# Optimization experiments

Hardware: AMD Instinct MI355X
Metric: run time of the kernel (lower is better)

Reference implementation:

```python
import jax, jax.numpy as jnp
import numpy as np
from jax import lax

N_CLS = 3
ALPHA = 2
NMS = True


def _make_level(key, B, A, D, H, W, P, counts):
    k1, k2, k3, k4, k5 = jax.random.split(key, 5)
    C = N_CLS * A
    logit = jax.random.normal(k1, (B, C, D, H, W), dtype=jnp.float32)
    # valid positive coords use d,h,w >= 1 so padded writes to (0,0,0,0) never collide
    a = jax.random.randint(k2, (B, P), 0, A)
    d = jax.random.randint(k3, (B, P), 1, D)
    h = jax.random.randint(k4, (B, P), 1, H)
    w = jax.random.randint(k5, (B, P), 1, W)
    labels = jax.random.randint(jax.random.fold_in(key, 7), (B, P), 0, N_CLS)
    valid = jnp.arange(P)[None, :] < jnp.asarray(counts)[:, None]  # [B,P]
    coord = jnp.stack([a, d, h, w], axis=-1)
    coord = jnp.where(valid[..., None], coord, -1).astype(jnp.int32)
    # ground-truth prob map: -1 = negative, class id (float) at positive voxels
    prob_gt = -jnp.ones((B, A, D, H, W), dtype=jnp.float32)
    cs = jnp.where(valid[..., None], coord, 0)
    b_idx = jnp.arange(B)[:, None]
    vals = jnp.where(valid, labels.astype(jnp.float32), -1.0)
    prob_gt = prob_gt.at[b_idx, cs[..., 0], cs[..., 1], cs[..., 2], cs[..., 3]].set(vals)
    return logit, prob_gt, coord


def setup_inputs() -> dict:
    key = jax.random.key(0)
    kA, kB = jax.random.split(key)
    logit0, prob_gt0, coord0 = _make_level(kA, 4, 3, 64, 64, 64, 128, [128, 64, 32, 0])
    logit1, prob_gt1, coord1 = _make_level(kB, 4, 3, 32, 32, 32, 128, [64, 16, 8, 128])
    weight_cls = jnp.array([1.0, 1.5, 2.0], dtype=jnp.float32)
    return {
        "logit0": logit0, "logit1": logit1,
        "prob_gt0": prob_gt0, "prob_gt1": prob_gt1,
        "coord0": coord0, "coord1": coord1,
        "weight_cls": weight_cls,
    }


def _level_loss(logit, prob_gt, coord_gt, weight_cls):
    B, C, D, H, W = logit.shape
    A = C // N_CLS
    logit = logit.reshape(B, N_CLS, A, D, H, W)
    logp = jax.nn.log_softmax(logit, axis=1)
    nll = -logp                      # [B,N_cls,A,D,H,W]
    prob = jnp.exp(logp)
    nll_neg = nll[:, 0]              # [B,A,D,H,W]
    prob_neg = prob[:, 0]
    negmask = (prob_gt == -1).astype(logit.dtype)
    if NMS:
        mp = lax.reduce_window(nll_neg, -jnp.inf, lax.max,
                               (1, 1, 3, 3, 3), (1, 1, 1, 1, 1),
                               [(0, 0), (0, 0), (1, 1), (1, 1), (1, 1)])
        negmask = negmask * lax.stop_gradient((mp == nll_neg).astype(logit.dtype))
    w_neg = (1.0 - lax.stop_gradient(prob_neg)) ** ALPHA * negmask
    loss_neg = jnp.sum(nll_neg * w_neg)
    count_neg = jnp.sum(w_neg)
    # positives: ragged coord gather, masked instead of per-sample python loop
    valid = coord_gt[:, :, 0] > -1                       # [B,P]
    c = jnp.where(valid[..., None], coord_gt, 0)         # safe coords
    a, d, h, w = c[..., 0], c[..., 1], c[..., 2], c[..., 3]
    b_idx = jnp.arange(B)[:, None]
    cls = prob_gt[b_idx, a, d, h, w].astype(jnp.int32)   # class id at positives
    cls = jnp.where(valid, cls, 0)
    p_t = prob[b_idx, cls, a, d, h, w]
    nll_t = nll[b_idx, cls, a, d, h, w]
    w_pos = ((1.0 - lax.stop_gradient(p_t)) ** ALPHA
             * weight_cls[cls] * valid.astype(logit.dtype))
    loss_pos = jnp.sum(nll_t * w_pos)
    count_pos = jnp.sum(w_pos)
    return loss_pos, loss_neg, count_pos, count_neg


def reference(logit0, logit1, prob_gt0, prob_gt1, coord0, coord1, weight_cls):
    lp0, ln0, cp0, cn0 = _level_loss(logit0, prob_gt0, coord0, weight_cls)
    lp1, ln1, cp1, cn1 = _level_loss(logit1, prob_gt1, coord1, weight_cls)
    return jnp.stack([lp0 + lp1, ln0 + ln1, cp0 + cp1, cn0 + cn1])
```

## Files before the change

### kernel.cpp

```cpp
#include <hip/hip_runtime.h>
#include <math.h>

#define NEG_INF (-INFINITY)

__device__ __forceinline__ float nll3(float l0, float l1, float l2) {
    float m = fmaxf(l0, fmaxf(l1, l2));
    float e0 = __expf(l0 - m);
    float e1 = __expf(l1 - m);
    float e2 = __expf(l2 - m);
    return __logf(e0 + e1 + e2) - (l0 - m);
}

template<int W, int NR, int TD, int D, int H>
__device__ void neg_strip_v(int uid, int lane,
                            const float* __restrict__ logit,
                            const float* __restrict__ pg,
                            float2* __restrict__ slot) {
    constexpr int LR = W / 4;
    constexpr int NG = 64 / LR;
    constexpr int NI = NR + 2;
    constexpr int HG = H / NR;
    constexpr int DT = D / TD;
    const int q = lane % LR;
    const int g = lane / LR;

    int t = uid;
    const int hg = t % HG; t /= HG;
    const int dt = t % DT; t /= DT;
    const int ba = t;
    const int a = ba % 3, b = ba / 3;
    const int h0 = hg * NR, d0 = dt * TD;

    const long S = (long)D * H * W;
    const float* lb  = logit + ((long)b * 9 + a) * S;
    const long  cs   = 3 * S;
    const float* pgb = pg + (long)ba * S;

    const int jrow = h0 - 1 + g;
    const bool hv = (jrow >= 0) && (jrow < H) && (g < NI);
    const int hcl = min(max(jrow, 0), H - 1);
    const int rowoff = hcl * W + 4 * q;
    const int prowoff = (h0 + min(g, NR - 1)) * W + 4 * q;

    float4 c0, c1v, c2, n0, n1, n2, pgn;
    bool dvc = (d0 - 1 >= 0);
    {
        const float* p = lb + (long)max(d0 - 1, 0) * (H * W) + rowoff;
        c0  = *(const float4*)(p);
        c1v = *(const float4*)(p + cs);
        c2  = *(const float4*)(p + 2 * cs);
    }

    float vm0[4], vm1[4], cc1[4], pgc[4];
#pragma unroll
    for (int i = 0; i < 4; ++i) {
        vm0[i] = NEG_INF; vm1[i] = NEG_INF; cc1[i] = 0.f; pgc[i] = 0.f;
    }

    float loss = 0.f, cnt = 0.f;

#pragma unroll
    for (int s = 0; s <= TD + 1; ++s) {
        const int d = d0 - 1 + s;
        const bool dvn = (s <= TD - 1) || (d + 1 < D);
        if (s <= TD) {
            const float* p = lb + (long)min(d + 1, D - 1) * (H * W) + rowoff;
            n0 = *(const float4*)(p);
            n1 = *(const float4*)(p + cs);
            n2 = *(const float4*)(p + 2 * cs);
            pgn = *(const float4*)(pgb + (long)min(max(d, 0), D - 1) * (H * W)
                                   + prowoff);
        }

        float nvv[4];
        {
            const bool vv = dvc && hv;
            nvv[0] = vv ? nll3(c0.x, c1v.x, c2.x) : NEG_INF;
            nvv[1] = vv ? nll3(c0.y, c1v.y, c2.y) : NEG_INF;
            nvv[2] = vv ? nll3(c0.z, c1v.z, c2.z) : NEG_INF;
            nvv[3] = vv ? nll3(c0.w, c1v.w, c2.w) : NEG_INF;
        }

        float le = __shfl(nvv[3], lane - 1);
        float re = __shfl(nvv[0], lane + 1);
        le = (q == 0)      ? NEG_INF : le;
        re = (q == LR - 1) ? NEG_INF : re;
        float rm[4];
        rm[0] = fmaxf(le,     fmaxf(nvv[0], nvv[1]));
        rm[1] = fmaxf(nvv[0], fmaxf(nvv[1], nvv[2]));
        rm[2] = fmaxf(nvv[1], fmaxf(nvv[2], nvv[3]));
        rm[3] = fmaxf(nvv[2], fmaxf(nvv[3], re));

        float rmA[4], rmB[4], ctr[4];
#pragma unroll
        for (int i = 0; i < 4; ++i) {
            rmA[i] = __shfl(rm[i],  lane + LR);
            rmB[i] = __shfl(rm[i],  lane + 2 * LR);
            ctr[i] = __shfl(nvv[i], lane + LR);
        }

#pragma unroll
        for (int i = 0; i < 4; ++i) {
            float hw2 = fmaxf(rm[i], fmaxf(rmA[i], rmB[i]));
            if (s >= 2 && g < NR && pgc[i] == -1.0f) {
                float mp = fmaxf(vm0[i], fmaxf(vm1[i], hw2));
                if (mp == cc1[i]) {
                    float pn = __expf(-cc1[i]);
                    float wn = (1.f - pn) * (1.f - pn);
                    loss += cc1[i] * wn;
                    cnt  += wn;
                }
            }
            vm0[i] = vm1[i]; vm1[i] = hw2; cc1[i] = ctr[i];
        }
        pgc[0] = pgn.x; pgc[1] = pgn.y; pgc[2] = pgn.z; pgc[3] = pgn.w;
        dvc = dvn;
        c0 = n0; c1v = n1; c2 = n2;
    }

#pragma unroll
    for (int off = 32; off > 0; off >>= 1) {
        loss += __shfl_down(loss, off);
        cnt  += __shfl_down(cnt, off);
    }
    if (lane == 0) slot[uid] = make_float2(loss, cnt);
}

__device__ void pos_wave8(int sub, int lane,
                          const float* __restrict__ logit,
                          const float* __restrict__ prob_gt,
                          const int* __restrict__ coord,
                          const float* __restrict__ wcls,
                          float2* __restrict__ slot,
                          int D, int H, int W) {
    const int A = 3, P = 128;
    const long S = (long)D * H * W;
    const int i = sub * 64 + lane;
    const int b = i / P;
    const int* c = coord + (long)i * 4;
    const int a = c[0];
    float loss = 0.f, cnt = 0.f;
    if (a > -1) {
        const int d = c[1], h = c[2], w = c[3];
        const long s = ((long)d * H + h) * W + w;
        const int cls = (int)prob_gt[((long)b * A + a) * S + s];
        const float* lp = logit + ((long)b * 3 * A + a) * S + s;
        float l0 = lp[0];
        float l1 = lp[(long)A * S];
        float l2 = lp[2L * A * S];
        float m = fmaxf(l0, fmaxf(l1, l2));
        float e0 = __expf(l0 - m);
        float e1 = __expf(l1 - m);
        float e2 = __expf(l2 - m);
        float lsum = __logf(e0 + e1 + e2);
        float lc = (cls == 0) ? l0 : ((cls == 1) ? l1 : l2);
        float lpc = (lc - m) - lsum;
        float pt = __expf(lpc);
        float wp = (1.f - pt) * (1.f - pt) * wcls[cls];
        loss = (-lpc) * wp;
        cnt = wp;
    }
#pragma unroll
    for (int off = 32; off > 0; off >>= 1) {
        loss += __shfl_down(loss, off);
        cnt  += __shfl_down(cnt, off);
    }
    if (lane == 0) *slot = make_float2(loss, cnt);
}

#define NW0 6144
#define NW1 768
#define NWP 16
#define NUNEG (NW0 + NW1)
#define TOTAL_WAVES (NW0 + NW1 + NWP)

__global__ __launch_bounds__(256)
void mega_kernel(const float* __restrict__ logit0,
                 const float* __restrict__ logit1,
                 const float* __restrict__ pg0,
                 const float* __restrict__ pg1,
                 const int* __restrict__ coord0,
                 const int* __restrict__ coord1,
                 const float* __restrict__ wcls,
                 float2* __restrict__ ws) {
    const int gw = blockIdx.x * 4 + (threadIdx.x >> 6);
    const int lane = threadIdx.x & 63;
    float2* wsneg = ws;
    float2* wspos = ws + NUNEG;
    if (gw < NW0) {
        neg_strip_v<64, 2, 4, 64, 64>(gw, lane, logit0, pg0, wsneg);
    } else if (gw < NW0 + NW1) {
        neg_strip_v<32, 4, 4, 32, 32>(gw - NW0, lane, logit1, pg1, wsneg + NW0);
    } else if (gw < NW0 + NW1 + 8) {
        const int sub = gw - NW0 - NW1;
        pos_wave8(sub, lane, logit0, pg0, coord0, wcls, wspos + sub, 64, 64, 64);
    } else if (gw < NW0 + NW1 + 16) {
        const int sub = gw - NW0 - NW1 - 8;
        pos_wave8(sub, lane, logit1, pg1, coord1, wcls, wspos + 8 + sub, 32, 32, 32);
    }
}

__global__ __launch_bounds__(1024)
void final_reduce(const float2* __restrict__ ws, float* __restrict__ out) {
    const float2* wsneg = ws;
    const float2* wspos = ws + NUNEG;
    float ln = 0.f, cn = 0.f, lp = 0.f, cp = 0.f;
    for (int i = threadIdx.x; i < NUNEG; i += 1024) {
        float2 v = wsneg[i]; ln += v.x; cn += v.y;
    }
    if (threadIdx.x < NWP) {
        float2 v = wspos[threadIdx.x]; lp = v.x; cp = v.y;
    }
#pragma unroll
    for (int off = 32; off > 0; off >>= 1) {
        ln += __shfl_down(ln, off); cn += __shfl_down(cn, off);
        lp += __shfl_down(lp, off); cp += __shfl_down(cp, off);
    }
    __shared__ float s[16][4];
    const int wv = threadIdx.x >> 6;
    if ((threadIdx.x & 63) == 0) {
        s[wv][0] = ln; s[wv][1] = cn; s[wv][2] = lp; s[wv][3] = cp;
    }
    __syncthreads();
    if (threadIdx.x == 0) {
        float a = 0.f, b = 0.f, c = 0.f, d = 0.f;
#pragma unroll
        for (int i = 0; i < 16; ++i) {
            a += s[i][0]; b += s[i][1]; c += s[i][2]; d += s[i][3];
        }
        out[0] = c;
        out[1] = a;
        out[2] = d;
        out[3] = b;
    }
}

extern "C" void kernel_launch(void* const* d_in, const int* in_sizes, int n_in,
                              void* d_out, int out_size, void* d_ws, size_t ws_size,
                              hipStream_t stream) {
    const float* logit0   = (const float*)d_in[0];
    const float* logit1   = (const float*)d_in[1];
    const float* prob_gt0 = (const float*)d_in[2];
    const float* prob_gt1 = (const float*)d_in[3];
    const int*   coord0   = (const int*)d_in[4];
    const int*   coord1   = (const int*)d_in[5];
    const float* wcls     = (const float*)d_in[6];
    float* out = (float*)d_out;
    float2* ws = (float2*)d_ws;

    mega_kernel<<<TOTAL_WAVES / 4, 256, 0, stream>>>(
        logit0, logit1, prob_gt0, prob_gt1, coord0, coord1, wcls, ws);
    final_reduce<<<1, 1024, 0, stream>>>(ws, out);
}
```

Measured before the change: 106.6 us.

## Deepen depth-slice prefetch to two slices and double depth tile per wave

The negative-loss strip kernel now keeps a three-stage register pipeline (current, next, next-next depth slices) so loads are issued two iterations ahead of use, and each wave processes 8 depth slices instead of 4, halving the wave count. This aims to hide global load latency better and amortize the halo slice reloads across more slices. It raises register pressure, which may reduce occupancy, and the final dispatch branch is made unconditional, which relies on the grid matching the wave total exactly.

```diff
diff --git a/kernel.cpp b/kernel.cpp
--- a/kernel.cpp
+++ b/kernel.cpp
@@ -12,12 +12,11 @@
 }
 
 template<int W, int NR, int TD, int D, int H>
-__device__ void neg_strip_v(int uid, int lane,
-                            const float* __restrict__ logit,
-                            const float* __restrict__ pg,
-                            float2* __restrict__ slot) {
+__device__ void neg_strip_p2(int uid, int lane,
+                             const float* __restrict__ logit,
+                             const float* __restrict__ pg,
+                             float2* __restrict__ slot) {
     constexpr int LR = W / 4;
-    constexpr int NG = 64 / LR;
     constexpr int NI = NR + 2;
     constexpr int HG = H / NR;
     constexpr int DT = D / TD;
@@ -30,8 +29,9 @@
     const int ba = t;
     const int a = ba % 3, b = ba / 3;
     const int h0 = hg * NR, d0 = dt * TD;
-
-    const long S = (long)D * H * W;
+    const int HW = H * W;
+
+    const long S = (long)D * HW;
     const float* lb  = logit + ((long)b * 9 + a) * S;
     const long  cs   = 3 * S;
     const float* pgb = pg + (long)ba * S;
@@ -42,43 +42,54 @@
     const int rowoff = hcl * W + 4 * q;
     const int prowoff = (h0 + min(g, NR - 1)) * W + 4 * q;
 
-    float4 c0, c1v, c2, n0, n1, n2, pgn;
-    bool dvc = (d0 - 1 >= 0);
+    float4 A0, A1, A2, B0, B1, B2, C0, C1, C2;
+    float4 GA, GB, GC;
+    bool vA, vB, vC;
+
     {
-        const float* p = lb + (long)max(d0 - 1, 0) * (H * W) + rowoff;
-        c0  = *(const float4*)(p);
-        c1v = *(const float4*)(p + cs);
-        c2  = *(const float4*)(p + 2 * cs);
-    }
-
-    float vm0[4], vm1[4], cc1[4], pgc[4];
-#pragma unroll
-    for (int i = 0; i < 4; ++i) {
-        vm0[i] = NEG_INF; vm1[i] = NEG_INF; cc1[i] = 0.f; pgc[i] = 0.f;
-    }
+        const float* p = lb + (long)max(d0 - 1, 0) * HW + rowoff;
+        A0 = *(const float4*)p;
+        A1 = *(const float4*)(p + cs);
+        A2 = *(const float4*)(p + 2 * cs);
+        vA = (d0 - 1 >= 0);
+        const float* p2 = lb + (long)d0 * HW + rowoff;
+        B0 = *(const float4*)p2;
+        B1 = *(const float4*)(p2 + cs);
+        B2 = *(const float4*)(p2 + 2 * cs);
+        vB = true;
+        GA = make_float4(0.f, 0.f, 0.f, 0.f);
+        GB = make_float4(0.f, 0.f, 0.f, 0.f);
+    }
+
+    float vm0[4], vm1[4], cc1[4];
+#pragma unroll
+    for (int i = 0; i < 4; ++i) { vm0[i] = NEG_INF; vm1[i] = NEG_INF; cc1[i] = 0.f; }
 
     float loss = 0.f, cnt = 0.f;
 
 #pragma unroll
     for (int s = 0; s <= TD + 1; ++s) {
-        const int d = d0 - 1 + s;
-        const bool dvn = (s <= TD - 1) || (d + 1 < D);
-        if (s <= TD) {
-            const float* p = lb + (long)min(d + 1, D - 1) * (H * W) + rowoff;
-            n0 = *(const float4*)(p);
-            n1 = *(const float4*)(p + cs);
-            n2 = *(const float4*)(p + 2 * cs);
-            pgn = *(const float4*)(pgb + (long)min(max(d, 0), D - 1) * (H * W)
-                                   + prowoff);
+        if (s <= TD - 1) {
+            const int pd = d0 + 1 + s;
+            const float* p = lb + (long)min(pd, D - 1) * HW + rowoff;
+            C0 = *(const float4*)p;
+            C1 = *(const float4*)(p + cs);
+            C2 = *(const float4*)(p + 2 * cs);
+            vC = (pd < D);
+            GC = *(const float4*)(pgb + (long)(d0 + s) * HW + prowoff);
+        } else {
+            vC = false;
+            C0 = C1 = C2 = make_float4(0.f, 0.f, 0.f, 0.f);
+            GC = make_float4(0.f, 0.f, 0.f, 0.f);
         }
 
         float nvv[4];
         {
-            const bool vv = dvc && hv;
-            nvv[0] = vv ? nll3(c0.x, c1v.x, c2.x) : NEG_INF;
-            nvv[1] = vv ? nll3(c0.y, c1v.y, c2.y) : NEG_INF;
-            nvv[2] = vv ? nll3(c0.z, c1v.z, c2.z) : NEG_INF;
-            nvv[3] = vv ? nll3(c0.w, c1v.w, c2.w) : NEG_INF;
+            const bool vv = vA && hv;
+            nvv[0] = vv ? nll3(A0.x, A1.x, A2.x) : NEG_INF;
+            nvv[1] = vv ? nll3(A0.y, A1.y, A2.y) : NEG_INF;
+            nvv[2] = vv ? nll3(A0.z, A1.z, A2.z) : NEG_INF;
+            nvv[3] = vv ? nll3(A0.w, A1.w, A2.w) : NEG_INF;
         }
 
         float le = __shfl(nvv[3], lane - 1);
@@ -99,10 +110,11 @@
             ctr[i] = __shfl(nvv[i], lane + LR);
         }
 
+        const float pgv[4] = {GA.x, GA.y, GA.z, GA.w};
 #pragma unroll
         for (int i = 0; i < 4; ++i) {
             float hw2 = fmaxf(rm[i], fmaxf(rmA[i], rmB[i]));
-            if (s >= 2 && g < NR && pgc[i] == -1.0f) {
+            if (s >= 2 && g < NR && pgv[i] == -1.0f) {
                 float mp = fmaxf(vm0[i], fmaxf(vm1[i], hw2));
                 if (mp == cc1[i]) {
                     float pn = __expf(-cc1[i]);
@@ -113,9 +125,10 @@
             }
             vm0[i] = vm1[i]; vm1[i] = hw2; cc1[i] = ctr[i];
         }
-        pgc[0] = pgn.x; pgc[1] = pgn.y; pgc[2] = pgn.z; pgc[3] = pgn.w;
-        dvc = dvn;
-        c0 = n0; c1v = n1; c2 = n2;
+
+        GA = GB; GB = GC;
+        A0 = B0; A1 = B1; A2 = B2; vA = vB;
+        B0 = C0; B1 = C1; B2 = C2; vB = vC;
     }
 
 #pragma unroll
@@ -168,8 +181,8 @@
     if (lane == 0) *slot = make_float2(loss, cnt);
 }
 
-#define NW0 6144
-#define NW1 768
+#define NW0 3072
+#define NW1 384
 #define NWP 16
 #define NUNEG (NW0 + NW1)
 #define TOTAL_WAVES (NW0 + NW1 + NWP)
@@ -188,13 +201,13 @@
     float2* wsneg = ws;
     float2* wspos = ws + NUNEG;
     if (gw < NW0) {
-        neg_strip_v<64, 2, 4, 64, 64>(gw, lane, logit0, pg0, wsneg);
+        neg_strip_p2<64, 2, 8, 64, 64>(gw, lane, logit0, pg0, wsneg);
     } else if (gw < NW0 + NW1) {
-        neg_strip_v<32, 4, 4, 32, 32>(gw - NW0, lane, logit1, pg1, wsneg + NW0);
+        neg_strip_p2<32, 4, 8, 32, 32>(gw - NW0, lane, logit1, pg1, wsneg + NW0);
     } else if (gw < NW0 + NW1 + 8) {
         const int sub = gw - NW0 - NW1;
         pos_wave8(sub, lane, logit0, pg0, coord0, wcls, wspos + sub, 64, 64, 64);
-    } else if (gw < NW0 + NW1 + 16) {
+    } else {
         const int sub = gw - NW0 - NW1 - 8;
         pos_wave8(sub, lane, logit1, pg1, coord1, wcls, wspos + 8 + sub, 32, 32, 32);
     }
```

Result: no change. 106.0 us (median of 2 runs) (-0.5%).
